# Optimization experiments

Hardware: AMD Instinct MI355X
Metric: run time of the kernel (lower is better)

The kernel has to match this reference:

```python
import jax, jax.numpy as jnp
import numpy as np

D_MODEL = 768
NUM_HEADS = 8
DEPTH = D_MODEL // NUM_HEADS


def setup_inputs() -> dict:
    key = jax.random.key(0)
    ks = jax.random.split(key, 12)
    B, S = 4, 2048
    s = 0.02
    return {
        "q_in": jax.random.normal(ks[0], (B, S, D_MODEL), jnp.float32),
        "k_in": jax.random.normal(ks[1], (B, S, D_MODEL), jnp.float32),
        "v_in": jax.random.normal(ks[2], (B, S, D_MODEL), jnp.float32),
        "mask": jnp.zeros((B, 1, 1, S), jnp.float32),
        "wq": jax.random.normal(ks[3], (D_MODEL, D_MODEL), jnp.float32) * s,
        "bq": jax.random.normal(ks[4], (D_MODEL,), jnp.float32) * s,
        "wk": jax.random.normal(ks[5], (D_MODEL, D_MODEL), jnp.float32) * s,
        "bk": jax.random.normal(ks[6], (D_MODEL,), jnp.float32) * s,
        "wv": jax.random.normal(ks[7], (D_MODEL, D_MODEL), jnp.float32) * s,
        "bv": jax.random.normal(ks[8], (D_MODEL,), jnp.float32) * s,
        "wo": jax.random.normal(ks[9], (D_MODEL, D_MODEL), jnp.float32) * s,
        "bo": jax.random.normal(ks[10], (D_MODEL,), jnp.float32) * s,
    }


def _split_heads(x, B):
    # [B, S, D] -> [B, H, S, depth]
    return x.reshape(B, -1, NUM_HEADS, DEPTH).transpose(0, 2, 1, 3)


def reference(q_in, k_in, v_in, mask, wq, bq, wk, bk, wv, bv, wo, bo):
    B = q_in.shape[0]
    q = _split_heads(q_in @ wq + bq, B)   # [B,H,Sq,d]
    k = _split_heads(k_in @ wk + bk, B)   # [B,H,Sk,d]
    v = _split_heads(v_in @ wv + bv, B)   # [B,H,Sk,d]

    scale = 1.0 / jnp.sqrt(jnp.float32(DEPTH))
    logits = jnp.einsum("bhqd,bhkd->bhqk", q, k) * scale
    logits = logits + mask * (-1e9)
    attn = jax.nn.softmax(logits, axis=-1)            # [B,H,Sq,Sk]
    ctx = jnp.einsum("bhqk,bhkd->bhqd", attn, v)
    ctx = ctx.transpose(0, 2, 1, 3).reshape(B, -1, D_MODEL)  # concat heads
    out = ctx @ wo + bo
    return out, attn
```

## Files before the change

### kernel.cpp

```cpp
#include <hip/hip_runtime.h>
#include <hip/hip_bf16.h>
#include <stdint.h>


#define SEQ 2048
#define DM 768
#define NB 4
#define NH 8
#define DEP 96
#define MROWS 8192

typedef __bf16 bf16x8 __attribute__((ext_vector_type(8)));
typedef float f32x4 __attribute__((ext_vector_type(4)));

__device__ inline unsigned short f2b(float f) {
    return __builtin_bit_cast(unsigned short, (__bf16)f);
}
__device__ inline bf16x8 ld_frag(const unsigned short* p) {
    return __builtin_bit_cast(bf16x8, *(const uint4*)p);
}
__device__ inline void gload_lds16(const unsigned short* g, unsigned short* l) {
    __builtin_amdgcn_global_load_lds(
        (const __attribute__((address_space(1))) unsigned int*)g,
        (__attribute__((address_space(3))) unsigned int*)l, 16, 0, 0);
}

__global__ __launch_bounds__(256) void wt_kernel(
    const float* __restrict__ w0, const float* __restrict__ w1,
    const float* __restrict__ w2, const float* __restrict__ w3,
    unsigned short* __restrict__ wt)
{
    __shared__ float tile[32][33];
    int mat = blockIdx.z;
    const float* w = mat == 0 ? w0 : mat == 1 ? w1 : mat == 2 ? w2 : w3;
    unsigned short* dst = wt + (size_t)mat * DM * DM;
    int k0 = blockIdx.x * 32, n0 = blockIdx.y * 32;
    int tx = threadIdx.x & 31, ty = threadIdx.x >> 5;
#pragma unroll
    for (int i = 0; i < 4; i++)
        tile[ty + i * 8][tx] = w[(size_t)(k0 + ty + i * 8) * DM + n0 + tx];
    __syncthreads();
#pragma unroll
    for (int i = 0; i < 4; i++)
        dst[(size_t)(n0 + ty + i * 8) * DM + k0 + tx] = f2b(tile[tx][ty + i * 8]);
}

__global__ __launch_bounds__(256) void xcvt_kernel(
    const float* __restrict__ q, const float* __restrict__ k, const float* __restrict__ v,
    unsigned short* __restrict__ xb)
{
    int z = blockIdx.z;
    const float* src = z == 0 ? q : z == 1 ? k : v;
    unsigned short* dst = xb + (size_t)z * MROWS * DM;
    size_t i = ((size_t)blockIdx.x * 256 + threadIdx.x) * 8;
    float4 f0 = *(const float4*)(src + i);
    float4 f1 = *(const float4*)(src + i + 4);
    bf16x8 p;
    p[0] = (__bf16)f0.x; p[1] = (__bf16)f0.y; p[2] = (__bf16)f0.z; p[3] = (__bf16)f0.w;
    p[4] = (__bf16)f1.x; p[5] = (__bf16)f1.y; p[6] = (__bf16)f1.z; p[7] = (__bf16)f1.w;
    *(uint4*)(dst + i) = __builtin_bit_cast(uint4, p);
}

__global__ __launch_bounds__(256) void proj_kernel(
    const unsigned short* __restrict__ xb, const unsigned short* __restrict__ wt,
    const float* __restrict__ bq, const float* __restrict__ bk, const float* __restrict__ bv,
    unsigned short* __restrict__ qb, unsigned short* __restrict__ kb, unsigned short* __restrict__ vb)
{
    __shared__ unsigned short As[128 * 32];
    __shared__ unsigned short Bs[128 * 32];

    int z = blockIdx.z;
    const unsigned short* x = xb + (size_t)z * MROWS * DM;
    const unsigned short* W = wt + (size_t)z * DM * DM;
    const float* bias = z == 0 ? bq : z == 1 ? bk : bv;
    unsigned short* out = z == 0 ? qb : z == 1 ? kb : vb;

    int tid = threadIdx.x;
    int lane = tid & 63, wv_ = tid >> 6;
    int col = lane & 15, quad = lane >> 4;
    int m0 = blockIdx.x * 128, n0 = blockIdx.y * 128;
    int mi = (wv_ & 1) * 64, ni = (wv_ >> 1) * 64;
    int sr = tid >> 2, so = (tid & 3) * 8;

    f32x4 acc[4][4] = {};
    for (int kk = 0; kk < DM; kk += 32) {
        __syncthreads();
        gload_lds16(x + (size_t)(m0 + sr) * DM + kk + so,      &As[tid * 8]);
        gload_lds16(x + (size_t)(m0 + 64 + sr) * DM + kk + so, &As[2048 + tid * 8]);
        gload_lds16(W + (size_t)(n0 + sr) * DM + kk + so,      &Bs[tid * 8]);
        gload_lds16(W + (size_t)(n0 + 64 + sr) * DM + kk + so, &Bs[2048 + tid * 8]);
        __syncthreads();
        bf16x8 af[4], bfr[4];
#pragma unroll
        for (int mt = 0; mt < 4; mt++)
            af[mt] = ld_frag(&As[(mi + mt * 16 + col) * 32 + quad * 8]);
#pragma unroll
        for (int nt = 0; nt < 4; nt++)
            bfr[nt] = ld_frag(&Bs[(ni + nt * 16 + col) * 32 + quad * 8]);
#pragma unroll
        for (int mt = 0; mt < 4; mt++)
#pragma unroll
            for (int nt = 0; nt < 4; nt++)
                acc[mt][nt] = __builtin_amdgcn_mfma_f32_16x16x32_bf16(af[mt], bfr[nt], acc[mt][nt], 0, 0, 0);
    }
#pragma unroll
    for (int mt = 0; mt < 4; mt++) {
        int grow_base = m0 + mi + mt * 16 + quad * 4;
#pragma unroll
        for (int nt = 0; nt < 4; nt++) {
            int gcol = n0 + ni + nt * 16 + col;
            float bv_ = bias[gcol];
            int h = gcol / DEP, d = gcol % DEP;
#pragma unroll
            for (int r = 0; r < 4; r++) {
                int grow = grow_base + r;
                int b = grow >> 11, s = grow & 2047;
                out[((size_t)((b * NH + h) * SEQ + s)) * DEP + d] = f2b(acc[mt][nt][r] + bv_);
            }
        }
    }
}

__global__ __launch_bounds__(256) void vt_kernel(
    const unsigned short* __restrict__ vb, unsigned short* __restrict__ vt)
{
    __shared__ unsigned short tile[32][33];
    int bh = blockIdx.z;
    int s0 = blockIdx.x * 32, d0 = blockIdx.y * 32;
    int tx = threadIdx.x & 31, ty = threadIdx.x >> 5;
    const unsigned short* src = vb + (size_t)bh * SEQ * DEP;
    unsigned short* dst = vt + (size_t)bh * DEP * SEQ;
#pragma unroll
    for (int i = 0; i < 4; i++)
        tile[ty + i * 8][tx] = src[(size_t)(s0 + ty + i * 8) * DEP + d0 + tx];
    __syncthreads();
#pragma unroll
    for (int i = 0; i < 4; i++)
        dst[(size_t)(d0 + ty + i * 8) * SEQ + s0 + tx] = tile[tx][ty + i * 8];
}

__global__ __launch_bounds__(256, 6) void attn_kernel(
    const unsigned short* __restrict__ qb, const unsigned short* __restrict__ kb,
    const unsigned short* __restrict__ vt, const float* __restrict__ mask,
    float* __restrict__ attn_out, unsigned short* __restrict__ ctx)
{
    __shared__ float mask_s[SEQ];
    __shared__ unsigned short p_lds[4][16 * 72];
    __shared__ float lsum_x[2][2][16];
    __shared__ f32x4 o_xchg[2][64];

    int tid = threadIdx.x;
    int w = tid >> 6, lane = tid & 63, col = lane & 15, quad = lane >> 4;
    int qg = w & 1, kh = w >> 1;

    int lin = blockIdx.y * gridDim.x + blockIdx.x;
    int nid = (lin & 7) * 256 + (lin >> 3);
    int bh = nid >> 6;
    int qblk = nid & 63;
    int b = bh >> 3, h = bh & 7;
    int q0 = qblk * 32 + qg * 16;
    int kbeg = kh * (SEQ / 2), kend = kbeg + SEQ / 2;

    const unsigned short* Qp = qb + (size_t)bh * SEQ * DEP;
    const unsigned short* Kp = kb + (size_t)bh * SEQ * DEP;
    const unsigned short* Vp = vt + (size_t)bh * DEP * SEQ;
    float* attn = attn_out + (size_t)bh * SEQ * SEQ;

    const float NLOG2E = -1.4426950408889634e9f;
    for (int i = tid; i < SEQ; i += 256)
        mask_s[i] = mask[b * SEQ + i] * NLOG2E;
    __syncthreads();

    bf16x8 aq[3];
#pragma unroll
    for (int ks = 0; ks < 3; ks++)
        aq[ks] = ld_frag(Qp + (size_t)(q0 + col) * DEP + ks * 32 + quad * 8);

    const float s2 = 0.10206207261596575f * 1.4426950408889634f;
    float lsum[4] = {0.f, 0.f, 0.f, 0.f};

    for (int kt = kbeg; kt < kend; kt += 64) {
#pragma unroll
        for (int nt = 0; nt < 4; nt++) {
            const unsigned short* kr = Kp + (size_t)(kt + nt * 16 + col) * DEP;
            f32x4 c = {0.f, 0.f, 0.f, 0.f};
#pragma unroll
            for (int ks = 0; ks < 3; ks++)
                c = __builtin_amdgcn_mfma_f32_16x16x32_bf16(aq[ks], ld_frag(kr + ks * 32 + quad * 8), c, 0, 0, 0);
            float mv = mask_s[kt + nt * 16 + col];
#pragma unroll
            for (int r = 0; r < 4; r++)
                lsum[r] += __builtin_amdgcn_exp2f(c[r] * s2 + mv);
        }
    }
#pragma unroll
    for (int r = 0; r < 4; r++) {
        float v = lsum[r];
        v += __shfl_xor(v, 1); v += __shfl_xor(v, 2);
        v += __shfl_xor(v, 4); v += __shfl_xor(v, 8);
        lsum[r] = v;
    }
    if (col == 0) {
#pragma unroll
        for (int r = 0; r < 4; r++)
            lsum_x[qg][kh][quad * 4 + r] = lsum[r];
    }
    __syncthreads();
#pragma unroll
    for (int r = 0; r < 4; r++)
        lsum[r] = 1.0f / (lsum_x[qg][0][quad * 4 + r] + lsum_x[qg][1][quad * 4 + r]);

    f32x4 o[6] = {};
    for (int kt = kbeg; kt < kend; kt += 64) {
#pragma unroll
        for (int nt = 0; nt < 4; nt++) {
            const unsigned short* kr = Kp + (size_t)(kt + nt * 16 + col) * DEP;
            f32x4 c = {0.f, 0.f, 0.f, 0.f};
#pragma unroll
            for (int ks = 0; ks < 3; ks++)
                c = __builtin_amdgcn_mfma_f32_16x16x32_bf16(aq[ks], ld_frag(kr + ks * 32 + quad * 8), c, 0, 0, 0);
            float mv = mask_s[kt + nt * 16 + col];
#pragma unroll
            for (int r = 0; r < 4; r++) {
                float p = __builtin_amdgcn_exp2f(c[r] * s2 + mv) * lsum[r];
                attn[(size_t)(q0 + quad * 4 + r) * SEQ + kt + nt * 16 + col] = p;
                p_lds[w][(quad * 4 + r) * 72 + nt * 16 + col] = f2b(p);
            }
        }
        bf16x8 pa0 = ld_frag(&p_lds[w][col * 72 + quad * 8]);
        bf16x8 pa1 = ld_frag(&p_lds[w][col * 72 + 32 + quad * 8]);
        const unsigned short* vbase = Vp + (size_t)col * SEQ + kt;
#pragma unroll
        for (int dt = 0; dt < 6; dt++) {
            const unsigned short* vr = vbase + (size_t)dt * 16 * SEQ;
            o[dt] = __builtin_amdgcn_mfma_f32_16x16x32_bf16(pa0, ld_frag(vr + quad * 8), o[dt], 0, 0, 0);
            o[dt] = __builtin_amdgcn_mfma_f32_16x16x32_bf16(pa1, ld_frag(vr + 32 + quad * 8), o[dt], 0, 0, 0);
        }
    }

#pragma unroll
    for (int dt = 0; dt < 6; dt++) {
        __syncthreads();
        if (kh == 1) o_xchg[qg][lane] = o[dt];
        __syncthreads();
        if (kh == 0) o[dt] += o_xchg[qg][lane];
    }
    if (kh == 0) {
#pragma unroll
        for (int dt = 0; dt < 6; dt++)
#pragma unroll
            for (int r = 0; r < 4; r++) {
                int qrow = q0 + quad * 4 + r;
                ctx[(size_t)(b * SEQ + qrow) * DM + h * DEP + dt * 16 + col] = f2b(o[dt][r]);
            }
    }
}

__global__ __launch_bounds__(256) void oproj_kernel(
    const unsigned short* __restrict__ ctx, const unsigned short* __restrict__ woT,
    const float* __restrict__ bo, float* __restrict__ out)
{
    __shared__ unsigned short As[128 * 32];
    __shared__ unsigned short Bs[128 * 32];

    int tid = threadIdx.x;
    int lane = tid & 63, wv_ = tid >> 6;
    int col = lane & 15, quad = lane >> 4;
    int m0 = blockIdx.x * 128, n0 = blockIdx.y * 128;
    int mi = (wv_ & 1) * 64, ni = (wv_ >> 1) * 64;
    int sr = tid >> 2, so = (tid & 3) * 8;

    f32x4 acc[4][4] = {};
    for (int kk = 0; kk < DM; kk += 32) {
        __syncthreads();
        gload_lds16(ctx + (size_t)(m0 + sr) * DM + kk + so,      &As[tid * 8]);
        gload_lds16(ctx + (size_t)(m0 + 64 + sr) * DM + kk + so, &As[2048 + tid * 8]);
        gload_lds16(woT + (size_t)(n0 + sr) * DM + kk + so,      &Bs[tid * 8]);
        gload_lds16(woT + (size_t)(n0 + 64 + sr) * DM + kk + so, &Bs[2048 + tid * 8]);
        __syncthreads();
        bf16x8 af[4], bfr[4];
#pragma unroll
        for (int mt = 0; mt < 4; mt++)
            af[mt] = ld_frag(&As[(mi + mt * 16 + col) * 32 + quad * 8]);
#pragma unroll
        for (int nt = 0; nt < 4; nt++)
            bfr[nt] = ld_frag(&Bs[(ni + nt * 16 + col) * 32 + quad * 8]);
#pragma unroll
        for (int mt = 0; mt < 4; mt++)
#pragma unroll
            for (int nt = 0; nt < 4; nt++)
                acc[mt][nt] = __builtin_amdgcn_mfma_f32_16x16x32_bf16(af[mt], bfr[nt], acc[mt][nt], 0, 0, 0);
    }
#pragma unroll
    for (int mt = 0; mt < 4; mt++) {
        int grow_base = m0 + mi + mt * 16 + quad * 4;
#pragma unroll
        for (int nt = 0; nt < 4; nt++) {
            int gcol = n0 + ni + nt * 16 + col;
            float bv_ = bo[gcol];
#pragma unroll
            for (int r = 0; r < 4; r++)
                out[(size_t)(grow_base + r) * DM + gcol] = acc[mt][nt][r] + bv_;
        }
    }
}

extern "C" void kernel_launch(void* const* d_in, const int* in_sizes, int n_in,
                              void* d_out, int out_size, void* d_ws, size_t ws_size,
                              hipStream_t stream) {
    (void)in_sizes; (void)n_in; (void)out_size; (void)ws_size;
    const float* q_in = (const float*)d_in[0];
    const float* k_in = (const float*)d_in[1];
    const float* v_in = (const float*)d_in[2];
    const float* mask = (const float*)d_in[3];
    const float* wq = (const float*)d_in[4];
    const float* bq = (const float*)d_in[5];
    const float* wk = (const float*)d_in[6];
    const float* bk = (const float*)d_in[7];
    const float* wv = (const float*)d_in[8];
    const float* bv = (const float*)d_in[9];
    const float* wo = (const float*)d_in[10];
    const float* bo = (const float*)d_in[11];

    unsigned short* ws = (unsigned short*)d_ws;
    const size_t WMAT = (size_t)DM * DM;
    const size_t QKV = (size_t)NB * NH * SEQ * DEP;
    unsigned short* wT    = ws;
    unsigned short* qbuf  = ws + 4 * WMAT;
    unsigned short* kbuf  = qbuf + QKV;
    unsigned short* vbuf  = kbuf + QKV;
    unsigned short* xb    = vbuf + QKV;
    unsigned short* vtbuf = xb;
    unsigned short* ctxbuf = xb + QKV;

    float* out_f = (float*)d_out;
    float* attn_f = out_f + (size_t)NB * SEQ * DM;

    dim3 blk(256);
    wt_kernel<<<dim3(24, 24, 4), blk, 0, stream>>>(wq, wk, wv, wo, wT);
    xcvt_kernel<<<dim3(3072, 1, 3), blk, 0, stream>>>(q_in, k_in, v_in, xb);
    proj_kernel<<<dim3(MROWS / 128, DM / 128, 3), blk, 0, stream>>>(
        xb, wT, bq, bk, bv, qbuf, kbuf, vbuf);
    vt_kernel<<<dim3(SEQ / 32, DEP / 32, NB * NH), blk, 0, stream>>>(vbuf, vtbuf);
    attn_kernel<<<dim3(SEQ / 32, NB * NH), blk, 0, stream>>>(
        qbuf, kbuf, vtbuf, mask, attn_f, ctxbuf);
    oproj_kernel<<<dim3(MROWS / 128, DM / 128), blk, 0, stream>>>(
        ctxbuf, wT + 3 * WMAT, bo, out_f);
}
```

Measured before the change: 1.204 ms.

## Double-buffer LDS tiles in projection GEMMs and relax attention launch bounds

The QKV projection and output projection GEMMs now keep two LDS buffers per operand. Each iteration issues the global-to-LDS loads for the next K-slice before the MFMAs on the current slice, using one barrier per iteration instead of two. This is meant to hide global load latency behind matrix math, at the cost of doubling the shared memory used by these kernels. Separately, the attention kernel's minimum-blocks hint drops from 6 to 4. That gives the compiler a larger register budget per thread, which may cut spills but can lower occupancy.

```diff
diff --git a/kernel.cpp b/kernel.cpp
--- a/kernel.cpp
+++ b/kernel.cpp
@@ -66,8 +66,8 @@
     const float* __restrict__ bq, const float* __restrict__ bk, const float* __restrict__ bv,
     unsigned short* __restrict__ qb, unsigned short* __restrict__ kb, unsigned short* __restrict__ vb)
 {
-    __shared__ unsigned short As[128 * 32];
-    __shared__ unsigned short Bs[128 * 32];
+    __shared__ unsigned short As[2][128 * 32];
+    __shared__ unsigned short Bs[2][128 * 32];
 
     int z = blockIdx.z;
     const unsigned short* x = xb + (size_t)z * MROWS * DM;
@@ -82,26 +82,40 @@
     int mi = (wv_ & 1) * 64, ni = (wv_ >> 1) * 64;
     int sr = tid >> 2, so = (tid & 3) * 8;
 
+    const unsigned short* xs0 = x + (size_t)(m0 + sr) * DM + so;
+    const unsigned short* xs1 = x + (size_t)(m0 + 64 + sr) * DM + so;
+    const unsigned short* ws0 = W + (size_t)(n0 + sr) * DM + so;
+    const unsigned short* ws1 = W + (size_t)(n0 + 64 + sr) * DM + so;
+
     f32x4 acc[4][4] = {};
-    for (int kk = 0; kk < DM; kk += 32) {
-        __syncthreads();
-        gload_lds16(x + (size_t)(m0 + sr) * DM + kk + so,      &As[tid * 8]);
-        gload_lds16(x + (size_t)(m0 + 64 + sr) * DM + kk + so, &As[2048 + tid * 8]);
-        gload_lds16(W + (size_t)(n0 + sr) * DM + kk + so,      &Bs[tid * 8]);
-        gload_lds16(W + (size_t)(n0 + 64 + sr) * DM + kk + so, &Bs[2048 + tid * 8]);
-        __syncthreads();
+    gload_lds16(xs0, &As[0][tid * 8]);
+    gload_lds16(xs1, &As[0][2048 + tid * 8]);
+    gload_lds16(ws0, &Bs[0][tid * 8]);
+    gload_lds16(ws1, &Bs[0][2048 + tid * 8]);
+    __syncthreads();
+
+    for (int t = 0; t < DM / 32; ++t) {
+        int cur = t & 1;
+        if (t < DM / 32 - 1) {
+            int kk = (t + 1) * 32;
+            gload_lds16(xs0 + kk, &As[cur ^ 1][tid * 8]);
+            gload_lds16(xs1 + kk, &As[cur ^ 1][2048 + tid * 8]);
+            gload_lds16(ws0 + kk, &Bs[cur ^ 1][tid * 8]);
+            gload_lds16(ws1 + kk, &Bs[cur ^ 1][2048 + tid * 8]);
+        }
         bf16x8 af[4], bfr[4];
 #pragma unroll
         for (int mt = 0; mt < 4; mt++)
-            af[mt] = ld_frag(&As[(mi + mt * 16 + col) * 32 + quad * 8]);
+            af[mt] = ld_frag(&As[cur][(mi + mt * 16 + col) * 32 + quad * 8]);
 #pragma unroll
         for (int nt = 0; nt < 4; nt++)
-            bfr[nt] = ld_frag(&Bs[(ni + nt * 16 + col) * 32 + quad * 8]);
+            bfr[nt] = ld_frag(&Bs[cur][(ni + nt * 16 + col) * 32 + quad * 8]);
 #pragma unroll
         for (int mt = 0; mt < 4; mt++)
 #pragma unroll
             for (int nt = 0; nt < 4; nt++)
                 acc[mt][nt] = __builtin_amdgcn_mfma_f32_16x16x32_bf16(af[mt], bfr[nt], acc[mt][nt], 0, 0, 0);
+        __syncthreads();
     }
 #pragma unroll
     for (int mt = 0; mt < 4; mt++) {
@@ -139,7 +153,7 @@
         dst[(size_t)(d0 + ty + i * 8) * SEQ + s0 + tx] = tile[tx][ty + i * 8];
 }
 
-__global__ __launch_bounds__(256, 6) void attn_kernel(
+__global__ __launch_bounds__(256, 4) void attn_kernel(
     const unsigned short* __restrict__ qb, const unsigned short* __restrict__ kb,
     const unsigned short* __restrict__ vt, const float* __restrict__ mask,
     float* __restrict__ attn_out, unsigned short* __restrict__ ctx)
@@ -260,8 +274,8 @@
     const unsigned short* __restrict__ ctx, const unsigned short* __restrict__ woT,
     const float* __restrict__ bo, float* __restrict__ out)
 {
-    __shared__ unsigned short As[128 * 32];
-    __shared__ unsigned short Bs[128 * 32];
+    __shared__ unsigned short As[2][128 * 32];
+    __shared__ unsigned short Bs[2][128 * 32];
 
     int tid = threadIdx.x;
     int lane = tid & 63, wv_ = tid >> 6;
@@ -270,26 +284,40 @@
     int mi = (wv_ & 1) * 64, ni = (wv_ >> 1) * 64;
     int sr = tid >> 2, so = (tid & 3) * 8;
 
+    const unsigned short* xs0 = ctx + (size_t)(m0 + sr) * DM + so;
+    const unsigned short* xs1 = ctx + (size_t)(m0 + 64 + sr) * DM + so;
+    const unsigned short* ws0 = woT + (size_t)(n0 + sr) * DM + so;
+    const unsigned short* ws1 = woT + (size_t)(n0 + 64 + sr) * DM + so;
+
     f32x4 acc[4][4] = {};
-    for (int kk = 0; kk < DM; kk += 32) {
-        __syncthreads();
-        gload_lds16(ctx + (size_t)(m0 + sr) * DM + kk + so,      &As[tid * 8]);
-        gload_lds16(ctx + (size_t)(m0 + 64 + sr) * DM + kk + so, &As[2048 + tid * 8]);
-        gload_lds16(woT + (size_t)(n0 + sr) * DM + kk + so,      &Bs[tid * 8]);
-        gload_lds16(woT + (size_t)(n0 + 64 + sr) * DM + kk + so, &Bs[2048 + tid * 8]);
-        __syncthreads();
+    gload_lds16(xs0, &As[0][tid * 8]);
+    gload_lds16(xs1, &As[0][2048 + tid * 8]);
+    gload_lds16(ws0, &Bs[0][tid * 8]);
+    gload_lds16(ws1, &Bs[0][2048 + tid * 8]);
+    __syncthreads();
+
+    for (int t = 0; t < DM / 32; ++t) {
+        int cur = t & 1;
+        if (t < DM / 32 - 1) {
+            int kk = (t + 1) * 32;
+            gload_lds16(xs0 + kk, &As[cur ^ 1][tid * 8]);
+            gload_lds16(xs1 + kk, &As[cur ^ 1][2048 + tid * 8]);
+            gload_lds16(ws0 + kk, &Bs[cur ^ 1][tid * 8]);
+            gload_lds16(ws1 + kk, &Bs[cur ^ 1][2048 + tid * 8]);
+        }
         bf16x8 af[4], bfr[4];
 #pragma unroll
         for (int mt = 0; mt < 4; mt++)
-            af[mt] = ld_frag(&As[(mi + mt * 16 + col) * 32 + quad * 8]);
+            af[mt] = ld_frag(&As[cur][(mi + mt * 16 + col) * 32 + quad * 8]);
 #pragma unroll
         for (int nt = 0; nt < 4; nt++)
-            bfr[nt] = ld_frag(&Bs[(ni + nt * 16 + col) * 32 + quad * 8]);
+            bfr[nt] = ld_frag(&Bs[cur][(ni + nt * 16 + col) * 32 + quad * 8]);
 #pragma unroll
         for (int mt = 0; mt < 4; mt++)
 #pragma unroll
             for (int nt = 0; nt < 4; nt++)
                 acc[mt][nt] = __builtin_amdgcn_mfma_f32_16x16x32_bf16(af[mt], bfr[nt], acc[mt][nt], 0, 0, 0);
+        __syncthreads();
     }
 #pragma unroll
     for (int mt = 0; mt < 4; mt++) {
```

New measurement: 1.041 ms. 1.16x faster.
